# Performance work log

Hardware: AMD Instinct MI355X
Metric: run time of the kernel (lower is better)

The kernel has to match this reference:

```python
import jax, jax.numpy as jnp
import numpy as np

B, S, D, H, DK, NQ, DFF = 4, 2048, 512, 8, 64, 4, 2048
EPS = 1e-5  # torch LayerNorm default


def setup_inputs() -> dict:
    key = jax.random.key(0)
    ks = jax.random.split(key, 8)
    sc = 1.0 / np.sqrt(D)
    inp = {"x": jax.random.normal(ks[0], (B, S, D), jnp.float32)}
    inp["wq"] = jax.random.normal(ks[1], (D, D), jnp.float32) * sc
    inp["bq"] = jnp.zeros((D,), jnp.float32)
    inp["wk"] = jax.random.normal(ks[2], (D, D), jnp.float32) * sc
    inp["bk"] = jnp.zeros((D,), jnp.float32)
    inp["wv"] = jax.random.normal(ks[3], (D, D), jnp.float32) * sc
    inp["bv"] = jnp.zeros((D,), jnp.float32)
    inp["wo"] = jax.random.normal(ks[4], (D, D), jnp.float32) * sc
    inp["bo"] = jnp.zeros((D,), jnp.float32)
    inp["w1"] = jax.random.normal(ks[5], (D, DFF), jnp.float32) * sc
    inp["b1"] = jnp.zeros((DFF,), jnp.float32)
    inp["w2"] = jax.random.normal(ks[6], (DFF, D), jnp.float32) * (1.0 / np.sqrt(DFF))
    inp["b2"] = jnp.zeros((D,), jnp.float32)
    inp["g1"] = jnp.ones((D,), jnp.float32)
    inp["be1"] = jnp.zeros((D,), jnp.float32)
    inp["g2"] = jnp.ones((D,), jnp.float32)
    inp["be2"] = jnp.zeros((D,), jnp.float32)
    return inp


def _layernorm(x, g, b):
    m = x.mean(-1, keepdims=True)
    v = ((x - m) ** 2).mean(-1, keepdims=True)
    return (x - m) * jax.lax.rsqrt(v + EPS) * g + b


def _forward(x, wq, bq, wk, bk, wv, bv, wo, bo, w1, b1, w2, b2, g1, be1, g2, be2):
    Bx, Sx, Dx = x.shape

    def heads(w, b):  # [B,S,D] -> [B,H,S,DK]
        return (x @ w + b).reshape(Bx, Sx, H, DK).transpose(0, 2, 1, 3)

    q, k, v = heads(wq, bq), heads(wk, bk), heads(wv, bv)
    # Quantum circuit 'execute' yields a uniform distribution over 2^NQ bitstrings,
    # so score = E_s[(qn.s)(kn.s)] = 0.25*(sum(qn)*sum(kn) + qn.kn) over the first
    # NQ components of each head slice (closed form of the original Python loops).
    qn, kn = q[..., :NQ], k[..., :NQ]
    scores = 0.25 * (
        qn.sum(-1)[..., :, None] * kn.sum(-1)[..., None, :]
        + jnp.einsum('bhin,bhjn->bhij', qn, kn)
    )
    attn = jax.nn.softmax(scores, axis=-1)  # [B,H,S,S]
    o = jnp.einsum('bhij,bhjd->bhid', attn, v)
    o = o.transpose(0, 2, 1, 3).reshape(Bx, Sx, Dx) @ wo + bo
    x1 = _layernorm(x + o, g1, be1)  # dropout is identity in eval
    ff = jax.nn.relu(x1 @ w1 + b1) @ w2 + b2
    return _layernorm(x1 + ff, g2, be2)


def reference(x, wq, bq, wk, bk, wv, bv, wo, bo, w1, b1, w2, b2, g1, be1, g2, be2):
    return _forward(x, wq, bq, wk, bk, wv, bv, wo, bo, w1, b1, w2, b2, g1, be1, g2, be2)
```

## Files before the change

### kernel.cpp

```cpp
#include <hip/hip_runtime.h>
#include <cstdint>

#define B_   4
#define S_   2048
#define D_   512
#define H_   8
#define DFF_ 2048

typedef __attribute__((ext_vector_type(4))) float  f32x4;
typedef __attribute__((ext_vector_type(4))) int    i32x4;
typedef __attribute__((ext_vector_type(2))) unsigned int u32x2;
typedef __attribute__((ext_vector_type(4))) unsigned int u32x4;
typedef __attribute__((ext_vector_type(8))) unsigned short u16x8;

#define VMCNT(n)    asm volatile("s_waitcnt vmcnt(" #n ")" ::: "memory")
#define BARRIER_RAW asm volatile("s_barrier" ::: "memory")

__device__ inline void mfma_bf16(f32x4& acc, i32x4 a, i32x4 b) {
  asm("v_mfma_f32_16x16x32_bf16 %0, %1, %2, %0" : "+v"(acc) : "v"(a), "v"(b));
}
__device__ inline unsigned cvt_pk_bf16(float lo, float hi) {
  unsigned r;
  asm("v_cvt_pk_bf16_f32 %0, %1, %2" : "=v"(r) : "v"(lo), "v"(hi));
  return r;
}
__device__ inline unsigned short f2b(float f) {
  unsigned u = __builtin_bit_cast(unsigned, f);
  u += 0x7fffu + ((u >> 16) & 1u);
  return (unsigned short)(u >> 16);
}
__device__ inline float b2f(unsigned short u) {
  return __builtin_bit_cast(float, ((unsigned)u) << 16);
}
__device__ inline void gload_lds16(const void* g, void* l) {
  __builtin_amdgcn_global_load_lds(
      (const __attribute__((address_space(1))) void*)g,
      (__attribute__((address_space(3))) void*)l, 16, 0, 0);
}
__device__ inline void gload_lds4(const void* g, void* l) {
  __builtin_amdgcn_global_load_lds(
      (const __attribute__((address_space(1))) void*)g,
      (__attribute__((address_space(3))) void*)l, 4, 0, 0);
}

__device__ inline void tconv_body(const float* __restrict__ src,
                                  unsigned short* __restrict__ dst,
                                  int RK, int CN, int bx, int by, int tid,
                                  float (*t)[65]) {
  const int tr0 = by * 64, tc0 = bx * 64;
  const int c4 = (tid & 15) * 4, rr = tid >> 4;
#pragma unroll
  for (int i = 0; i < 4; ++i) {
    int r = i * 16 + rr;
    f32x4 v = *(const f32x4*)(src + (size_t)(tr0 + r) * CN + tc0 + c4);
    t[r][c4] = v[0]; t[r][c4 + 1] = v[1]; t[r][c4 + 2] = v[2]; t[r][c4 + 3] = v[3];
  }
  __syncthreads();
#pragma unroll
  for (int i = 0; i < 4; ++i) {
    int oc = i * 16 + rr;
    unsigned lo = cvt_pk_bf16(t[c4][oc], t[c4 + 1][oc]);
    unsigned hi = cvt_pk_bf16(t[c4 + 2][oc], t[c4 + 3][oc]);
    u32x2 pk = {lo, hi};
    *(u32x2*)(dst + (size_t)(tc0 + oc) * RK + tr0 + c4) = pk;
  }
}

__global__ __launch_bounds__(256) void prep_kernel(
    const float* __restrict__ x,
    const float* __restrict__ wq, const float* __restrict__ bq,
    const float* __restrict__ wk, const float* __restrict__ bk,
    const float* __restrict__ wv, const float* __restrict__ bv,
    const float* __restrict__ wo,
    const float* __restrict__ w1, const float* __restrict__ w2,
    unsigned short* __restrict__ xb, unsigned short* __restrict__ wvb,
    unsigned short* __restrict__ wob, unsigned short* __restrict__ w1b,
    unsigned short* __restrict__ w2b, unsigned short* __restrict__ wqkb,
    float* __restrict__ biasv2) {
  __shared__ float tsh[64][65];
  const int blk = blockIdx.x, tid = threadIdx.x;
  if (blk < 2048) {
    size_t i = ((size_t)blk * 256 + tid) * 8;
    f32x4 a = *(const f32x4*)(x + i);
    f32x4 b = *(const f32x4*)(x + i + 4);
    u32x4 o = {cvt_pk_bf16(a[0], a[1]), cvt_pk_bf16(a[2], a[3]),
               cvt_pk_bf16(b[0], b[1]), cvt_pk_bf16(b[2], b[3])};
    *(u32x4*)(xb + i) = o;
  } else if (blk < 2112) {
    int c = blk - 2048;
    const float* w; const float* bb; int scol;
    if (c < 32) { w = wq; bb = bq; scol = (c >> 2) * 64 + (c & 3); }
    else { int c2 = c - 32; w = wk; bb = bk; scol = (c2 >> 2) * 64 + (c2 & 3); }
    for (int k = tid; k < 512; k += 256)
      wqkb[c * 512 + k] = f2b(w[(size_t)k * 512 + scol]);
    if (tid == 0) biasv2[512 + c] = bb[scol];
  } else if (blk < 2176) {
    int lb = blk - 2112;
    tconv_body(wv, wvb, 512, 512, lb & 7, lb >> 3, tid, tsh);
  } else if (blk < 2240) {
    int lb = blk - 2176;
    tconv_body(wo, wob, 512, 512, lb & 7, lb >> 3, tid, tsh);
  } else if (blk < 2496) {
    int lb = blk - 2240;
    tconv_body(w1, w1b, 512, 2048, lb & 31, lb >> 5, tid, tsh);
  } else if (blk < 2752) {
    int lb = blk - 2496;
    tconv_body(w2, w2b, 2048, 512, lb & 7, lb >> 3, tid, tsh);
  } else {
    int i = (blk - 2752) * 256 + tid;
    biasv2[i] = bv[i];
  }
}

template<int WM, int WN, int FM, int FN, int EPI>
__global__ __launch_bounds__(256) void gemm_kernel(
    const unsigned short* __restrict__ A, const unsigned short* __restrict__ Bt,
    const float* __restrict__ bias, void* __restrict__ Cout,
    void* __restrict__ Cout2, int M, int N, int K) {
  constexpr int BM = WM * FM * 16, BN = WN * FN * 16;
  constexpr int ACH = BM * 4, TCH = (BM + BN) * 4;
  constexpr int NS = TCH / 256;
  constexpr int BUFSZ = (BM + BN) * 64;
  __shared__ alignas(16) char lds[3][BUFSZ];
  const int tid = threadIdx.x, lane = tid & 63;
  const int wv = tid >> 6, wr = wv / WN, wc = wv % WN;
  const int bm0 = blockIdx.y * BM, bn0 = blockIdx.x * BN;
  const int l16 = lane & 15, lg = lane >> 4;

  auto stage = [&](int buf, int k0) {
#pragma unroll
    for (int i = 0; i < NS; ++i) {
      int ci = i * 256 + tid;
      const unsigned short* src;
      if (ci < ACH) {
        int r = ci >> 2, gs = ci & 3, g = gs ^ ((r >> 1) & 3);
        src = A + (size_t)(bm0 + r) * K + k0 + g * 8;
      } else {
        int cj = ci - ACH;
        int r = cj >> 2, gs = cj & 3, g = gs ^ ((r >> 1) & 3);
        src = Bt + (size_t)(bn0 + r) * K + k0 + g * 8;
      }
      gload_lds16(src, &lds[buf][ci * 16]);
    }
  };

  f32x4 acc[FM][FN];
#pragma unroll
  for (int i = 0; i < FM; ++i)
#pragma unroll
    for (int j = 0; j < FN; ++j) acc[i][j] = (f32x4){0.f, 0.f, 0.f, 0.f};

  const int T = K >> 5;
  stage(0, 0);
  if (T > 1) stage(1, 32);
  if constexpr (NS == 2) VMCNT(2); else if constexpr (NS == 3) VMCNT(3); else VMCNT(4);
  BARRIER_RAW;

  for (int t = 0; t < T; ++t) {
    const int cur = t % 3;
    const bool more = (t + 2 < T);
    if (more) stage((t + 2) % 3, (t + 2) << 5);

    i32x4 af[FM], bf[FN];
#pragma unroll
    for (int fm = 0; fm < FM; ++fm) {
      int r = wr * FM * 16 + fm * 16 + l16;
      int gs = lg ^ ((r >> 1) & 3);
      af[fm] = *(const i32x4*)(&lds[cur][r * 64 + gs * 16]);
    }
#pragma unroll
    for (int fn = 0; fn < FN; ++fn) {
      int r = wc * FN * 16 + fn * 16 + l16;
      int gs = lg ^ ((r >> 1) & 3);
      bf[fn] = *(const i32x4*)(&lds[cur][BM * 64 + r * 64 + gs * 16]);
    }
    __builtin_amdgcn_s_setprio(1);
#pragma unroll
    for (int fm = 0; fm < FM; ++fm)
#pragma unroll
      for (int fn = 0; fn < FN; ++fn)
        mfma_bf16(acc[fm][fn], af[fm], bf[fn]);
    __builtin_amdgcn_s_setprio(0);

    if (more) {
      if constexpr (NS == 2) VMCNT(2); else if constexpr (NS == 3) VMCNT(3); else VMCNT(4);
    } else {
      VMCNT(0);
    }
    BARRIER_RAW;
  }

#pragma unroll
  for (int fm = 0; fm < FM; ++fm) {
#pragma unroll
    for (int fn = 0; fn < FN; ++fn) {
      f32x4 a = acc[fm][fn];
      int gm = bm0 + wr * FM * 16 + fm * 16 + lg * 4;
      int gn = bn0 + wc * FN * 16 + fn * 16 + l16;
      float bz = bias[gn];
      if constexpr (EPI == 0) {
        float* C = (float*)Cout;
#pragma unroll
        for (int r = 0; r < 4; ++r) C[(size_t)(gm + r) * N + gn] = a[r] + bz;
      } else if constexpr (EPI == 1 || EPI == 2) {
        unsigned short* C = (unsigned short*)Cout;
#pragma unroll
        for (int r = 0; r < 4; ++r) {
          float v = a[r] + bz;
          if constexpr (EPI == 2) v = fmaxf(v, 0.f);
          C[(size_t)(gm + r) * N + gn] = f2b(v);
        }
      } else {
        if (gn < 512) {
          unsigned short* C = (unsigned short*)Cout;
          int b = gm >> 11, s = gm & 2047;
          int h = gn >> 6, d = gn & 63;
          u32x2 pk = {cvt_pk_bf16(a[0] + bz, a[1] + bz),
                      cvt_pk_bf16(a[2] + bz, a[3] + bz)};
          *(u32x2*)(C + (((size_t)(b * 8 + h)) * 64 + d) * 2048 + s) = pk;
        } else {
          float* qtp = (float*)Cout2;
          int c = (gn - 512) & 31, hh = c >> 2, nn = c & 3;
#pragma unroll
          for (int r = 0; r < 4; ++r) {
            float v = a[r] + bz;
            float s4 = v + __shfl_xor(v, 1);
            s4 += __shfl_xor(s4, 2);
            int gmr = gm + r, bb = gmr >> 11, ss = gmr & 2047;
            size_t oi = (((size_t)(bb * 8 + hh)) * 2048 + ss) * 4 + nn;
            if (gn < 544) qtp[oi] = 0.25f * v;
            else          qtp[262144 + oi] = v + s4;
          }
        }
      }
    }
  }
}

__global__ __launch_bounds__(256) void attn_kernel(
    const float* __restrict__ qt, const float* __restrict__ kh,
    const unsigned short* __restrict__ vt, unsigned short* __restrict__ O) {
  __shared__ alignas(16) char vlds[3][8192];
  __shared__ alignas(16) float khlds[3][256];
  const int tid = threadIdx.x, lane = tid & 63, wv = tid >> 6;
  const int L = blockIdx.x;
  const int x8 = L & 7, r8 = L >> 3;
  const int bh = x8 + 8 * (r8 & 3), qblk = r8 >> 2;
  const int b = bh >> 3, h = bh & 7;
  const int i0 = qblk * 64;
  const int l16 = lane & 15, g = lane >> 4;
  const int qrow = i0 + wv * 16 + l16;
  const float4 q = *(const float4*)(qt + ((size_t)bh * 2048 + qrow) * 4);
  const float* khb = kh + (size_t)bh * 2048 * 4;
  const unsigned short* vtb = vt + (size_t)bh * 64 * 2048;

  auto stage = [&](int buf, int j0) {
#pragma unroll
    for (int i = 0; i < 2; ++i) {
      int ci = i * 256 + tid;
      int d = ci >> 3, gs = ci & 7, gg = gs ^ (d & 7);
      gload_lds16(vtb + (size_t)d * 2048 + j0 + gg * 8, &vlds[buf][ci * 16]);
    }
    gload_lds4(khb + (size_t)j0 * 4 + tid, &khlds[buf][tid]);
  };

  f32x4 acc[4];
#pragma unroll
  for (int i = 0; i < 4; ++i) acc[i] = (f32x4){0.f, 0.f, 0.f, 0.f};
  float lsum = 0.f;

  stage(0, 0);
  stage(1, 64);
  VMCNT(3);
  BARRIER_RAW;

  for (int t = 0; t < 32; ++t) {
    const int cur = t % 3;
    const bool more = (t + 2 < 32);
    if (more) stage((t + 2) % 3, (t + 2) * 64);

#pragma unroll
    for (int ks = 0; ks < 2; ++ks) {
      float p[8];
#pragma unroll
      for (int jj = 0; jj < 8; ++jj) {
        f32x4 kv = *(const f32x4*)&khlds[cur][(ks * 32 + g * 8 + jj) * 4];
        float s = q.x * kv[0] + q.y * kv[1] + q.z * kv[2] + q.w * kv[3];
        p[jj] = __expf(s);
        lsum += p[jj];
      }
      i32x4 pb = {(int)cvt_pk_bf16(p[0], p[1]), (int)cvt_pk_bf16(p[2], p[3]),
                  (int)cvt_pk_bf16(p[4], p[5]), (int)cvt_pk_bf16(p[6], p[7])};
      __builtin_amdgcn_s_setprio(1);
#pragma unroll
      for (int dt = 0; dt < 4; ++dt) {
        int d = dt * 16 + l16;
        int gg = (ks * 4 + g) ^ (d & 7);
        i32x4 av = *(const i32x4*)(&vlds[cur][d * 128 + gg * 16]);
        mfma_bf16(acc[dt], av, pb);
      }
      __builtin_amdgcn_s_setprio(0);
    }

    if (more) VMCNT(3); else VMCNT(0);
    BARRIER_RAW;
  }

  lsum += __shfl_xor(lsum, 16);
  lsum += __shfl_xor(lsum, 32);
  const float rin = __fdividef(1.f, lsum);
  unsigned short* ob = O + ((size_t)(b * 2048 + qrow)) * 512 + h * 64;
#pragma unroll
  for (int dt = 0; dt < 4; ++dt) {
    f32x4 o = acc[dt] * rin;
    u32x2 pk = {cvt_pk_bf16(o[0], o[1]), cvt_pk_bf16(o[2], o[3])};
    *(u32x2*)(ob + dt * 16 + g * 4) = pk;
  }
}

__global__ __launch_bounds__(256) void ln1_kernel(const float* __restrict__ x,
                                                  const unsigned short* __restrict__ ob,
                                                  const float* __restrict__ g,
                                                  const float* __restrict__ be,
                                                  unsigned short* __restrict__ x1b) {
  const int row = blockIdx.x * 4 + (threadIdx.x >> 6), lane = threadIdx.x & 63;
  const float* xr = x + (size_t)row * 512 + lane * 8;
  f32x4 a0 = *(const f32x4*)xr, a1 = *(const f32x4*)(xr + 4);
  u16x8 rb = *(const u16x8*)(ob + (size_t)row * 512 + lane * 8);
  float v[8];
#pragma unroll
  for (int i = 0; i < 4; ++i) v[i] = a0[i] + b2f(rb[i]);
#pragma unroll
  for (int i = 0; i < 4; ++i) v[4 + i] = a1[i] + b2f(rb[4 + i]);
  float sum = 0.f;
#pragma unroll
  for (int i = 0; i < 8; ++i) sum += v[i];
#pragma unroll
  for (int m = 1; m < 64; m <<= 1) sum += __shfl_xor(sum, m);
  const float mean = sum * (1.f / 512.f);
  float vs = 0.f;
#pragma unroll
  for (int i = 0; i < 8; ++i) { v[i] -= mean; vs += v[i] * v[i]; }
#pragma unroll
  for (int m = 1; m < 64; m <<= 1) vs += __shfl_xor(vs, m);
  const float rs = rsqrtf(vs * (1.f / 512.f) + 1e-5f);
  const f32x4 g0 = *(const f32x4*)(g + lane * 8), g1 = *(const f32x4*)(g + lane * 8 + 4);
  const f32x4 b0 = *(const f32x4*)(be + lane * 8), b1 = *(const f32x4*)(be + lane * 8 + 4);
  float o[8];
#pragma unroll
  for (int i = 0; i < 4; ++i) o[i] = v[i] * rs * g0[i] + b0[i];
#pragma unroll
  for (int i = 0; i < 4; ++i) o[4 + i] = v[4 + i] * rs * g1[i] + b1[i];
  u32x4 pk = {cvt_pk_bf16(o[0], o[1]), cvt_pk_bf16(o[2], o[3]),
              cvt_pk_bf16(o[4], o[5]), cvt_pk_bf16(o[6], o[7])};
  *(u32x4*)(x1b + (size_t)row * 512 + lane * 8) = pk;
}

__global__ __launch_bounds__(256) void ln2_kernel(const unsigned short* __restrict__ x1b,
                                                  float* __restrict__ io,
                                                  const float* __restrict__ g,
                                                  const float* __restrict__ be) {
  const int row = blockIdx.x * 4 + (threadIdx.x >> 6), lane = threadIdx.x & 63;
  float* r = io + (size_t)row * 512 + lane * 8;
  f32x4 a0 = *(const f32x4*)r, a1 = *(const f32x4*)(r + 4);
  u16x8 rb = *(const u16x8*)(x1b + (size_t)row * 512 + lane * 8);
  float v[8];
#pragma unroll
  for (int i = 0; i < 4; ++i) v[i] = a0[i] + b2f(rb[i]);
#pragma unroll
  for (int i = 0; i < 4; ++i) v[4 + i] = a1[i] + b2f(rb[4 + i]);
  float sum = 0.f;
#pragma unroll
  for (int i = 0; i < 8; ++i) sum += v[i];
#pragma unroll
  for (int m = 1; m < 64; m <<= 1) sum += __shfl_xor(sum, m);
  const float mean = sum * (1.f / 512.f);
  float vs = 0.f;
#pragma unroll
  for (int i = 0; i < 8; ++i) { v[i] -= mean; vs += v[i] * v[i]; }
#pragma unroll
  for (int m = 1; m < 64; m <<= 1) vs += __shfl_xor(vs, m);
  const float rs = rsqrtf(vs * (1.f / 512.f) + 1e-5f);
  const f32x4 g0 = *(const f32x4*)(g + lane * 8), g1 = *(const f32x4*)(g + lane * 8 + 4);
  const f32x4 b0 = *(const f32x4*)(be + lane * 8), b1 = *(const f32x4*)(be + lane * 8 + 4);
  f32x4 o0, o1;
#pragma unroll
  for (int i = 0; i < 4; ++i) o0[i] = v[i] * rs * g0[i] + b0[i];
#pragma unroll
  for (int i = 0; i < 4; ++i) o1[i] = v[4 + i] * rs * g1[i] + b1[i];
  *(f32x4*)r = o0;
  *(f32x4*)(r + 4) = o1;
}

extern "C" void kernel_launch(void* const* d_in, const int* in_sizes, int n_in,
                              void* d_out, int out_size, void* d_ws, size_t ws_size,
                              hipStream_t stream) {
  const float* x   = (const float*)d_in[0];
  const float* wq  = (const float*)d_in[1];
  const float* bq  = (const float*)d_in[2];
  const float* wk  = (const float*)d_in[3];
  const float* bk  = (const float*)d_in[4];
  const float* wv  = (const float*)d_in[5];
  const float* bv  = (const float*)d_in[6];
  const float* wo  = (const float*)d_in[7];
  const float* bo  = (const float*)d_in[8];
  const float* w1  = (const float*)d_in[9];
  const float* b1  = (const float*)d_in[10];
  const float* w2  = (const float*)d_in[11];
  const float* b2  = (const float*)d_in[12];
  const float* g1  = (const float*)d_in[13];
  const float* be1 = (const float*)d_in[14];
  const float* g2  = (const float*)d_in[15];
  const float* be2 = (const float*)d_in[16];
  float* out = (float*)d_out;
  char* ws = (char*)d_ws;

  unsigned short* wvb    = (unsigned short*)(ws + 0x000000);
  unsigned short* wqkb   = (unsigned short*)(ws + 0x080000);
  float*          biasv2 = (float*)         (ws + 0x090000);
  unsigned short* wob    = (unsigned short*)(ws + 0x0A0000);
  unsigned short* w1b    = (unsigned short*)(ws + 0x120000);
  unsigned short* w2b    = (unsigned short*)(ws + 0x320000);
  float*          qt     = (float*)         (ws + 0x520000);
  float*          kh     = (float*)         (ws + 0x620000);
  unsigned short* x1b    = (unsigned short*)(ws + 0x720000);
  unsigned short* xb     = (unsigned short*)(ws + 0xF20000);
  unsigned short* Ob     = (unsigned short*)(ws + 0xF20000);
  unsigned short* hidden = (unsigned short*)(ws + 0xF20000);
  unsigned short* vtb    = (unsigned short*)(ws + 0x1720000);
  unsigned short* oprojb = (unsigned short*)(ws + 0x1720000);

  prep_kernel<<<2754, 256, 0, stream>>>(x, wq, bq, wk, bk, wv, bv, wo, w1, w2,
                                        xb, wvb, wob, w1b, w2b, wqkb, biasv2);

  gemm_kernel<2, 2, 4, 2, 5><<<dim3(9, 64), 256, 0, stream>>>(
      xb, wvb, biasv2, vtb, qt, 8192, 576, 512);

  attn_kernel<<<1024, 256, 0, stream>>>(qt, kh, vtb, Ob);

  gemm_kernel<2, 2, 4, 2, 1><<<dim3(8, 64), 256, 0, stream>>>(
      Ob, wob, bo, oprojb, nullptr, 8192, 512, 512);

  ln1_kernel<<<2048, 256, 0, stream>>>(x, oprojb, g1, be1, x1b);

  for (int c = 0; c < 2; ++c) {
    const unsigned short* x1c = x1b + (size_t)c * 4096 * 512;
    float* outc = out + (size_t)c * 4096 * 512;
    gemm_kernel<2, 2, 4, 4, 2><<<dim3(16, 32), 256, 0, stream>>>(
        x1c, w1b, b1, hidden, nullptr, 4096, 2048, 512);
    gemm_kernel<2, 2, 4, 2, 0><<<dim3(8, 32), 256, 0, stream>>>(
        hidden, w2b, b2, outc, nullptr, 4096, 512, 2048);
  }

  ln2_kernel<<<2048, 256, 0, stream>>>(x1b, out, g2, be2);
}
```

Measured before the change: 190.0 us.

## Split attention over key halves and combine partial outputs in a new kernel

Splits the attention key range into two halves, doubling the attention grid to 2048 blocks. Each half writes its unnormalized bf16 partial output and row sums, and a new combine kernel adds the two partials and normalizes. The aim is more parallelism and occupancy on the attention kernel. The cost is an extra launch, extra global traffic for the partial outputs, and an extra bf16 rounding of the unnormalized partials before combining.

```diff
diff --git a/kernel.cpp b/kernel.cpp
--- a/kernel.cpp
+++ b/kernel.cpp
@@ -239,15 +239,20 @@
 
 __global__ __launch_bounds__(256) void attn_kernel(
     const float* __restrict__ qt, const float* __restrict__ kh,
-    const unsigned short* __restrict__ vt, unsigned short* __restrict__ O) {
+    const unsigned short* __restrict__ vt,
+    unsigned short* __restrict__ O1, unsigned short* __restrict__ O2,
+    float* __restrict__ lsums) {
   __shared__ alignas(16) char vlds[3][8192];
   __shared__ alignas(16) float khlds[3][256];
   const int tid = threadIdx.x, lane = tid & 63, wv = tid >> 6;
   const int L = blockIdx.x;
   const int x8 = L & 7, r8 = L >> 3;
-  const int bh = x8 + 8 * (r8 & 3), qblk = r8 >> 2;
+  const int bh = x8 + 8 * (r8 & 3);
+  const int rest = r8 >> 2;
+  const int qblk = rest >> 1, half = rest & 1;
   const int b = bh >> 3, h = bh & 7;
   const int i0 = qblk * 64;
+  const int kbase = half * 1024;
   const int l16 = lane & 15, g = lane >> 4;
   const int qrow = i0 + wv * 16 + l16;
   const float4 q = *(const float4*)(qt + ((size_t)bh * 2048 + qrow) * 4);
@@ -269,15 +274,15 @@
   for (int i = 0; i < 4; ++i) acc[i] = (f32x4){0.f, 0.f, 0.f, 0.f};
   float lsum = 0.f;
 
-  stage(0, 0);
-  stage(1, 64);
+  stage(0, kbase);
+  stage(1, kbase + 64);
   VMCNT(3);
   BARRIER_RAW;
 
-  for (int t = 0; t < 32; ++t) {
+  for (int t = 0; t < 16; ++t) {
     const int cur = t % 3;
-    const bool more = (t + 2 < 32);
-    if (more) stage((t + 2) % 3, (t + 2) * 64);
+    const bool more = (t + 2 < 16);
+    if (more) stage((t + 2) % 3, kbase + (t + 2) * 64);
 
 #pragma unroll
     for (int ks = 0; ks < 2; ++ks) {
@@ -308,14 +313,33 @@
 
   lsum += __shfl_xor(lsum, 16);
   lsum += __shfl_xor(lsum, 32);
-  const float rin = __fdividef(1.f, lsum);
-  unsigned short* ob = O + ((size_t)(b * 2048 + qrow)) * 512 + h * 64;
+  if (g == 0)
+    lsums[half * 65536 + bh * 2048 + qrow] = lsum;
+  unsigned short* ob = (half ? O2 : O1) + ((size_t)(b * 2048 + qrow)) * 512 + h * 64;
 #pragma unroll
   for (int dt = 0; dt < 4; ++dt) {
-    f32x4 o = acc[dt] * rin;
+    f32x4 o = acc[dt];
     u32x2 pk = {cvt_pk_bf16(o[0], o[1]), cvt_pk_bf16(o[2], o[3])};
     *(u32x2*)(ob + dt * 16 + g * 4) = pk;
   }
+}
+
+__global__ __launch_bounds__(256) void comb_kernel(
+    unsigned short* __restrict__ O1, const unsigned short* __restrict__ O2,
+    const float* __restrict__ lsums) {
+  const int idx = blockIdx.x * 256 + threadIdx.x;
+  const int r = idx >> 6, j = idx & 63;
+  const int b = r >> 11, s = r & 2047, h = j >> 3;
+  const int li = (b * 8 + h) * 2048 + s;
+  const float rin = __fdividef(1.f, lsums[li] + lsums[65536 + li]);
+  u16x8 a = *(const u16x8*)(O1 + (size_t)r * 512 + j * 8);
+  u16x8 c = *(const u16x8*)(O2 + (size_t)r * 512 + j * 8);
+  float o[8];
+#pragma unroll
+  for (int i = 0; i < 8; ++i) o[i] = (b2f(a[i]) + b2f(c[i])) * rin;
+  u32x4 pk = {cvt_pk_bf16(o[0], o[1]), cvt_pk_bf16(o[2], o[3]),
+              cvt_pk_bf16(o[4], o[5]), cvt_pk_bf16(o[6], o[7])};
+  *(u32x4*)(O1 + (size_t)r * 512 + j * 8) = pk;
 }
 
 __global__ __launch_bounds__(256) void ln1_kernel(const float* __restrict__ x,
@@ -423,12 +447,14 @@
   unsigned short* w2b    = (unsigned short*)(ws + 0x320000);
   float*          qt     = (float*)         (ws + 0x520000);
   float*          kh     = (float*)         (ws + 0x620000);
+  unsigned short* O2     = (unsigned short*)(ws + 0x720000);
   unsigned short* x1b    = (unsigned short*)(ws + 0x720000);
   unsigned short* xb     = (unsigned short*)(ws + 0xF20000);
-  unsigned short* Ob     = (unsigned short*)(ws + 0xF20000);
+  unsigned short* O1     = (unsigned short*)(ws + 0xF20000);
   unsigned short* hidden = (unsigned short*)(ws + 0xF20000);
   unsigned short* vtb    = (unsigned short*)(ws + 0x1720000);
   unsigned short* oprojb = (unsigned short*)(ws + 0x1720000);
+  float*          lsums  = (float*)         (ws + 0x1F20000);
 
   prep_kernel<<<2754, 256, 0, stream>>>(x, wq, bq, wk, bk, wv, bv, wo, w1, w2,
                                         xb, wvb, wob, w1b, w2b, wqkb, biasv2);
@@ -436,10 +462,11 @@
   gemm_kernel<2, 2, 4, 2, 5><<<dim3(9, 64), 256, 0, stream>>>(
       xb, wvb, biasv2, vtb, qt, 8192, 576, 512);
 
-  attn_kernel<<<1024, 256, 0, stream>>>(qt, kh, vtb, Ob);
+  attn_kernel<<<2048, 256, 0, stream>>>(qt, kh, vtb, O1, O2, lsums);
+  comb_kernel<<<2048, 256, 0, stream>>>(O1, O2, lsums);
 
   gemm_kernel<2, 2, 4, 2, 1><<<dim3(8, 64), 256, 0, stream>>>(
-      Ob, wob, bo, oprojb, nullptr, 8192, 512, 512);
+      O1, wob, bo, oprojb, nullptr, 8192, 512, 512);
 
   ln1_kernel<<<2048, 256, 0, stream>>>(x, oprojb, g1, be1, x1b);
 
```

After: 192.3 us. Within noise of the previous version (+1.2%).
